# Optimization experiments

Measured on AMD Instinct MI355X. Metric: run time of the kernel, lower is better.

## Reference

```python
import jax, jax.numpy as jnp
import numpy as np

BN_EPS = 1e-5
MIN_DIST = 1e-10


def _conv_bn_relu(x, w, b, gamma, beta):
    # pointwise Conv1d (kernel=1) == per-point linear, then BatchNorm1d (training-mode
    # batch stats, biased variance, as torch does for normalization), then ReLU.
    y = jnp.einsum('oc,bcn->bon', w, x) + b[None, :, None]
    mu = y.mean(axis=(0, 2))
    var = y.var(axis=(0, 2))
    yn = (y - mu[None, :, None]) * jax.lax.rsqrt(var + BN_EPS)[None, :, None]
    return jax.nn.relu(yn * gamma[None, :, None] + beta[None, :, None])


def setup_inputs() -> dict:
    key = jax.random.key(0)
    ks = jax.random.split(key, 12)
    B, N1, N2, C1, C2 = 8, 8192, 2048, 128, 256
    in_ch = C1 + C2  # 384
    mlp = [256, 128]
    inp = {
        'xyz1': jax.random.normal(ks[0], (B, N1, 3), jnp.float32),
        'xyz2': jax.random.normal(ks[1], (B, N2, 3), jnp.float32),
        'points1': jax.random.normal(ks[2], (B, C1, N1), jnp.float32),
        'points2': jax.random.normal(ks[3], (B, C2, N2), jnp.float32),
    }
    last = in_ch
    for i, out_ch in enumerate(mlp):
        scale = 1.0 / np.sqrt(last)
        inp[f'w{i}'] = jax.random.uniform(ks[4 + 2 * i], (out_ch, last), jnp.float32, -scale, scale)
        inp[f'b{i}'] = jax.random.uniform(ks[5 + 2 * i], (out_ch,), jnp.float32, -scale, scale)
        inp[f'gamma{i}'] = jnp.ones((out_ch,), jnp.float32)
        inp[f'beta{i}'] = jnp.zeros((out_ch,), jnp.float32)
        last = out_ch
    return inp


def reference(xyz1, xyz2, points1, points2,
              w0, b0, gamma0, beta0, w1, b1, gamma1, beta1):
    # Euclidean distance matrix [B, N1, N2] (torch.cdist, p=2)
    sq = (jnp.sum(xyz1 * xyz1, -1)[:, :, None]
          + jnp.sum(xyz2 * xyz2, -1)[:, None, :]
          - 2.0 * jnp.einsum('bnd,bmd->bnm', xyz1, xyz2))
    dists = jnp.sqrt(jnp.maximum(sq, 0.0))
    # 3 smallest distances + indices (ascending, matching torch.topk largest=False)
    neg_d, knn_idx = jax.lax.top_k(-dists, 3)  # [B, N1, 3]
    knn_d = jnp.maximum(-neg_d, MIN_DIST)
    weights = 1.0 / knn_d
    weights = weights / jnp.sum(weights, axis=2, keepdims=True)  # [B, N1, 3]
    # gather neighbor features: points2 [B, C2, N2] -> [B, C2, N1, 3]
    knn_feats = jnp.take_along_axis(points2[:, :, None, :],
                                    knn_idx[:, None, :, :], axis=3)
    interpolated = jnp.sum(knn_feats * weights[:, None, :, :], axis=3)  # [B, C2, N1]
    new_points = jnp.concatenate([points1, interpolated], axis=1)  # [B, C1+C2, N1]
    new_points = _conv_bn_relu(new_points, w0, b0, gamma0, beta0)
    new_points = _conv_bn_relu(new_points, w1, b1, gamma1, beta1)
    return new_points
```

## Files before the change

### kernel.cpp

```cpp
#include <hip/hip_runtime.h>
#include <cstdint>

using u16 = unsigned short;
typedef short bf16x8 __attribute__((ext_vector_type(8)));
typedef float f32x4 __attribute__((ext_vector_type(4)));

__device__ __forceinline__ float bf2f(u16 h) {
    union { unsigned u; float f; } x;
    x.u = ((unsigned)h) << 16;
    return x.f;
}
__device__ __forceinline__ u16 f2bf(float f) {
    union { float f; unsigned u; } x;
    x.f = f;
    unsigned r = x.u + 0x7fffu + ((x.u >> 16) & 1u);
    return (u16)(r >> 16);
}

__global__ __launch_bounds__(256) void cvt_f32_bf16(const float* __restrict__ src,
                                                    u16* __restrict__ dst, int n) {
    int i = blockIdx.x * 256 + threadIdx.x;
    if (i < n) dst[i] = f2bf(src[i]);
}

__global__ __launch_bounds__(256) void transpose_to_bf16(const float* __restrict__ src,
                                                         u16* __restrict__ dst,
                                                         int C, int N, int dst_stride,
                                                         int col_off) {
    __shared__ float tile[32][33];
    int b = blockIdx.z;
    int n0 = blockIdx.x * 32, c0 = blockIdx.y * 32;
    int tx = threadIdx.x & 31, ty = threadIdx.x >> 5;
    const float* s = src + (long)b * C * N;
#pragma unroll
    for (int i = 0; i < 4; i++) {
        int c = ty + i * 8;
        tile[c][tx] = s[(long)(c0 + c) * N + n0 + tx];
    }
    __syncthreads();
    u16* d = dst + (long)b * N * dst_stride;
#pragma unroll
    for (int i = 0; i < 4; i++) {
        int n = ty + i * 8;
        d[(long)(n0 + n) * dst_stride + col_off + c0 + tx] = f2bf(tile[tx][n]);
    }
}

#define N1 8192
#define N2 2048
#define C2 256

__global__ __launch_bounds__(256) void knn_interp(const float* __restrict__ xyz1,
                                                  const float* __restrict__ xyz2,
                                                  const u16* __restrict__ P2T,
                                                  u16* __restrict__ X) {
    __shared__ float4 pts[N2];
    __shared__ float m_d[4][64][3];
    __shared__ int   m_i[4][64][3];
    __shared__ int   s_idx[64][3];
    __shared__ float s_w[64][3];
    int b = blockIdx.y;
    int n0 = blockIdx.x * 64;
    int tid = threadIdx.x;
    int ql = tid & 63;
    int part = tid >> 6;

    for (int j = tid; j < N2; j += 256) {
        float x = xyz2[((long)b * N2 + j) * 3 + 0];
        float y = xyz2[((long)b * N2 + j) * 3 + 1];
        float z = xyz2[((long)b * N2 + j) * 3 + 2];
        float nsq = __fadd_rn(__fadd_rn(__fmul_rn(x, x), __fmul_rn(y, y)), __fmul_rn(z, z));
        pts[j] = make_float4(x, y, z, nsq);
    }
    __syncthreads();

    int n = n0 + ql;
    float px = xyz1[((long)b * N1 + n) * 3 + 0];
    float py = xyz1[((long)b * N1 + n) * 3 + 1];
    float pz = xyz1[((long)b * N1 + n) * 3 + 2];
    float psq = __fadd_rn(__fadd_rn(__fmul_rn(px, px), __fmul_rn(py, py)), __fmul_rn(pz, pz));

    float b0 = 1e30f, b1 = 1e30f, b2 = 1e30f;
    int i0 = 0, i1 = 0, i2 = 0;
    int jbeg = part * (N2 / 4);
#pragma unroll 8
    for (int jj = 0; jj < N2 / 4; jj++) {
        int j = jbeg + jj;
        float4 p = pts[j];
        float dot = __fadd_rn(__fadd_rn(__fmul_rn(px, p.x), __fmul_rn(py, p.y)),
                              __fmul_rn(pz, p.z));
        float sq = __fsub_rn(__fadd_rn(psq, p.w), __fmul_rn(2.0f, dot));
        if (sq < b2) {
            if (sq < b1) {
                b2 = b1; i2 = i1;
                if (sq < b0) { b1 = b0; i1 = i0; b0 = sq; i0 = j; }
                else         { b1 = sq; i1 = j; }
            } else { b2 = sq; i2 = j; }
        }
    }
    m_d[part][ql][0] = b0; m_d[part][ql][1] = b1; m_d[part][ql][2] = b2;
    m_i[part][ql][0] = i0; m_i[part][ql][1] = i1; m_i[part][ql][2] = i2;
    __syncthreads();

    if (tid < 64) {
        float c0 = 1e30f, c1 = 1e30f, c2 = 1e30f;
        int a0 = 0x7fffffff, a1 = 0x7fffffff, a2 = 0x7fffffff;
#pragma unroll
        for (int pp = 0; pp < 4; pp++) {
#pragma unroll
            for (int k = 0; k < 3; k++) {
                float d = m_d[pp][tid][k];
                int ix = m_i[pp][tid][k];
                if (d < c2 || (d == c2 && ix < a2)) {
                    if (d < c1 || (d == c1 && ix < a1)) {
                        c2 = c1; a2 = a1;
                        if (d < c0 || (d == c0 && ix < a0)) { c1 = c0; a1 = a0; c0 = d; a0 = ix; }
                        else                                { c1 = d; a1 = ix; }
                    } else { c2 = d; a2 = ix; }
                }
            }
        }
        float e0 = sqrtf(fmaxf(c0, 0.0f));
        float e1 = sqrtf(fmaxf(c1, 0.0f));
        float e2 = sqrtf(fmaxf(c2, 0.0f));
        float kd0 = fmaxf(e0, 1e-10f), kd1 = fmaxf(e1, 1e-10f), kd2 = fmaxf(e2, 1e-10f);
        float w0 = __fdiv_rn(1.0f, kd0), w1 = __fdiv_rn(1.0f, kd1), w2 = __fdiv_rn(1.0f, kd2);
        float wsum = __fadd_rn(__fadd_rn(w0, w1), w2);
        s_idx[tid][0] = a0; s_idx[tid][1] = a1; s_idx[tid][2] = a2;
        s_w[tid][0] = __fdiv_rn(w0, wsum);
        s_w[tid][1] = __fdiv_rn(w1, wsum);
        s_w[tid][2] = __fdiv_rn(w2, wsum);
    }
    __syncthreads();

    int l = tid & 63;
    const u16* base = P2T + (long)b * N2 * C2;
    for (int p = part; p < 64; p += 4) {
        int j0 = s_idx[p][0], j1 = s_idx[p][1], j2 = s_idx[p][2];
        float f0 = s_w[p][0], f1 = s_w[p][1], f2 = s_w[p][2];
        ushort4 r0 = *(const ushort4*)&base[(long)j0 * C2 + l * 4];
        ushort4 r1 = *(const ushort4*)&base[(long)j1 * C2 + l * 4];
        ushort4 r2 = *(const ushort4*)&base[(long)j2 * C2 + l * 4];
        ushort4 o;
        {
            float acc = __fadd_rn(__fadd_rn(__fmul_rn(bf2f(r0.x), f0), __fmul_rn(bf2f(r1.x), f1)),
                                  __fmul_rn(bf2f(r2.x), f2));
            o.x = f2bf(acc);
        }
        {
            float acc = __fadd_rn(__fadd_rn(__fmul_rn(bf2f(r0.y), f0), __fmul_rn(bf2f(r1.y), f1)),
                                  __fmul_rn(bf2f(r2.y), f2));
            o.y = f2bf(acc);
        }
        {
            float acc = __fadd_rn(__fadd_rn(__fmul_rn(bf2f(r0.z), f0), __fmul_rn(bf2f(r1.z), f1)),
                                  __fmul_rn(bf2f(r2.z), f2));
            o.z = f2bf(acc);
        }
        {
            float acc = __fadd_rn(__fadd_rn(__fmul_rn(bf2f(r0.w), f0), __fmul_rn(bf2f(r1.w), f1)),
                                  __fmul_rn(bf2f(r2.w), f2));
            o.w = f2bf(acc);
        }
        *(ushort4*)&X[(long)(b * N1 + n0 + p) * 384 + 128 + l * 4] = o;
    }
}

template <int KDIM, bool BN_IN, bool OUT_BF16>
__global__ __launch_bounds__(256) void gemm_bn(const u16* __restrict__ A,
                                               const u16* __restrict__ Bw,
                                               const float* __restrict__ bias,
                                               const float* __restrict__ g_in_sum,
                                               const float* __restrict__ g_in_ssq,
                                               const float* __restrict__ gamma_in,
                                               const float* __restrict__ beta_in,
                                               void* __restrict__ Yout, int Ntot,
                                               float* __restrict__ g_out_sum,
                                               float* __restrict__ g_out_ssq) {
    __shared__ __align__(16) u16 Al[128 * 40];
    __shared__ __align__(16) u16 Bl[128 * 40];
    __shared__ float s_stats[256];
    __shared__ float s_scale[BN_IN ? KDIM : 2];
    __shared__ float s_shift[BN_IN ? KDIM : 2];

    int tid = threadIdx.x;
    long s0 = (long)blockIdx.x * 128;
    int o0 = blockIdx.y * 128;

    s_stats[tid < 256 ? tid : 0] = 0.0f;
    if constexpr (BN_IN) {
        for (int k = tid; k < KDIM; k += 256) {
            float mu = g_in_sum[k] * (1.0f / 65536.0f);
            float var = g_in_ssq[k] * (1.0f / 65536.0f) - mu * mu;
            float rs = rsqrtf(var + 1e-5f);
            float sc = gamma_in[k] * rs;
            s_scale[k] = sc;
            s_shift[k] = beta_in[k] - mu * sc;
        }
    }
    int wid = tid >> 6, lane = tid & 63;
    int wm = wid >> 1, wn = wid & 1;
    int q = lane >> 4, l16 = lane & 15;

    f32x4 acc[4][4];
#pragma unroll
    for (int mi = 0; mi < 4; mi++)
#pragma unroll
        for (int ni = 0; ni < 4; ni++) acc[mi][ni] = (f32x4){0.f, 0.f, 0.f, 0.f};
    __syncthreads();

    for (int kt = 0; kt < KDIM; kt += 32) {
#pragma unroll
        for (int cc = 0; cc < 2; cc++) {
            int ci = tid + cc * 256;
            int row = ci >> 2;
            int kc = (ci & 3) << 3;
            union { uint4 u; u16 h[8]; } va;
            va.u = *(const uint4*)(A + (s0 + row) * KDIM + kt + kc);
            if constexpr (BN_IN) {
#pragma unroll
                for (int j = 0; j < 8; j++) {
                    float f = bf2f(va.h[j]);
                    f = fmaxf(fmaf(f, s_scale[kt + kc + j], s_shift[kt + kc + j]), 0.0f);
                    va.h[j] = f2bf(f);
                }
            }
            *(uint4*)&Al[row * 40 + kc] = va.u;
            *(uint4*)&Bl[row * 40 + kc] = *(const uint4*)(Bw + (long)(o0 + row) * KDIM + kt + kc);
        }
        __syncthreads();
        bf16x8 af[4], bfr[4];
#pragma unroll
        for (int mi = 0; mi < 4; mi++)
            af[mi] = *(const bf16x8*)&Al[(wm * 64 + mi * 16 + l16) * 40 + q * 8];
#pragma unroll
        for (int ni = 0; ni < 4; ni++)
            bfr[ni] = *(const bf16x8*)&Bl[(wn * 64 + ni * 16 + l16) * 40 + q * 8];
#pragma unroll
        for (int mi = 0; mi < 4; mi++)
#pragma unroll
            for (int ni = 0; ni < 4; ni++)
                acc[mi][ni] = __builtin_amdgcn_mfma_f32_16x16x32_bf16(af[mi], bfr[ni],
                                                                      acc[mi][ni], 0, 0, 0);
        __syncthreads();
    }

#pragma unroll
    for (int ni = 0; ni < 4; ni++) {
        int coll = wn * 64 + ni * 16 + l16;
        int col = o0 + coll;
        float bz = bias[col];
        float s1 = 0.0f, s2 = 0.0f;
#pragma unroll
        for (int mi = 0; mi < 4; mi++) {
#pragma unroll
            for (int r = 0; r < 4; r++) {
                float v = acc[mi][ni][r] + bz;
                s1 += v;
                s2 += v * v;
                long row = s0 + wm * 64 + mi * 16 + q * 4 + r;
                if constexpr (OUT_BF16)
                    ((u16*)Yout)[row * Ntot + col] = f2bf(v);
                else
                    ((float*)Yout)[row * Ntot + col] = v;
            }
        }
        s1 += __shfl_xor(s1, 16, 64);
        s1 += __shfl_xor(s1, 32, 64);
        s2 += __shfl_xor(s2, 16, 64);
        s2 += __shfl_xor(s2, 32, 64);
        if (q == 0) {
            atomicAdd(&s_stats[coll], s1);
            atomicAdd(&s_stats[128 + coll], s2);
        }
    }
    __syncthreads();
    if (tid < 128) {
        atomicAdd(&g_out_sum[o0 + tid], s_stats[tid]);
        atomicAdd(&g_out_ssq[o0 + tid], s_stats[128 + tid]);
    }
}

__global__ __launch_bounds__(256) void finalize_k(const float* __restrict__ Y1,
                                                  const float* __restrict__ g_sum,
                                                  const float* __restrict__ g_ssq,
                                                  const float* __restrict__ gamma,
                                                  const float* __restrict__ beta,
                                                  float* __restrict__ out) {
    __shared__ float s_scale[128], s_shift[128];
    int tid = threadIdx.x;
    if (tid < 128) {
        float mu = g_sum[tid] * (1.0f / 65536.0f);
        float var = g_ssq[tid] * (1.0f / 65536.0f) - mu * mu;
        float rs = rsqrtf(var + 1e-5f);
        float sc = gamma[tid] * rs;
        s_scale[tid] = sc;
        s_shift[tid] = beta[tid] - mu * sc;
    }
    __syncthreads();
    long s = (long)blockIdx.x * 256 + tid;
    int b = (int)(s >> 13);
    int n = (int)(s & 8191);
    const float* yrow = Y1 + s * 128;
    float* obase = out + (long)b * 128 * 8192 + n;
#pragma unroll 8
    for (int o = 0; o < 128; o++) {
        float v = fmaxf(fmaf(yrow[o], s_scale[o], s_shift[o]), 0.0f);
        obase[(long)o * 8192] = v;
    }
}

extern "C" void kernel_launch(void* const* d_in, const int* in_sizes, int n_in,
                              void* d_out, int out_size, void* d_ws, size_t ws_size,
                              hipStream_t stream) {
    const float* xyz1   = (const float*)d_in[0];
    const float* xyz2   = (const float*)d_in[1];
    const float* points1 = (const float*)d_in[2];
    const float* points2 = (const float*)d_in[3];
    const float* w0 = (const float*)d_in[4];
    const float* b0 = (const float*)d_in[5];
    const float* gamma0 = (const float*)d_in[6];
    const float* beta0 = (const float*)d_in[7];
    const float* w1 = (const float*)d_in[8];
    const float* b1 = (const float*)d_in[9];
    const float* gamma1 = (const float*)d_in[10];
    const float* beta1 = (const float*)d_in[11];
    float* out = (float*)d_out;

    char* ws = (char*)d_ws;
    u16* X    = (u16*)(ws + 0);
    u16* P2T  = (u16*)(ws + 50331648);
    u16* w0b  = (u16*)(ws + 58720256);
    u16* w1b  = (u16*)(ws + 58916864);
    u16* Y0   = (u16*)(ws + 58982400);
    float* Y1 = (float*)(ws + 92536832);
    float* stats = (float*)(ws + 126091264);
    if (ws_size < 126094336) return;
    float* gsum0 = stats;
    float* gss0  = stats + 256;
    float* gsum1 = stats + 512;
    float* gss1  = stats + 640;

    hipMemsetAsync(stats, 0, 768 * sizeof(float), stream);
    cvt_f32_bf16<<<384, 256, 0, stream>>>(w0, w0b, 98304);
    cvt_f32_bf16<<<128, 256, 0, stream>>>(w1, w1b, 32768);
    transpose_to_bf16<<<dim3(256, 4, 8), 256, 0, stream>>>(points1, X, 128, 8192, 384, 0);
    transpose_to_bf16<<<dim3(64, 8, 8), 256, 0, stream>>>(points2, P2T, 256, 2048, 256, 0);
    knn_interp<<<dim3(128, 8), 256, 0, stream>>>(xyz1, xyz2, P2T, X);
    gemm_bn<384, false, true><<<dim3(512, 2), 256, 0, stream>>>(
        X, w0b, b0, nullptr, nullptr, nullptr, nullptr, Y0, 256, gsum0, gss0);
    gemm_bn<256, true, false><<<dim3(512, 1), 256, 0, stream>>>(
        Y0, w1b, b1, gsum0, gss0, gamma0, beta0, Y1, 128, gsum1, gss1);
    finalize_k<<<256, 256, 0, stream>>>(Y1, gsum1, gss1, gamma1, beta1, out);
}
```

Baseline: 281.9 us.

## Fuse prep kernels, precompute xyz2 norms, widen KNN blocks, store Y1 as bf16

Merges the weight conversions, the stats memset and a new xyz2 preprocessing step (pre-scaled coordinates plus squared norm) into one prep kernel. The KNN kernel now reads that precomputed array from global memory instead of staging it in LDS. It uses 512 threads split into 8 parts and replaces the branchy top-3 insert with branchless selects. The second GEMM writes bf16 instead of fp32, and finalize reads it with vectorized loads, which halves the intermediate traffic at some cost in precision.

Result: no change. 284.8 us (+1.0%).

```diff
diff --git a/kernel.cpp b/kernel.cpp
--- a/kernel.cpp
+++ b/kernel.cpp
@@ -17,10 +17,32 @@
     return (u16)(r >> 16);
 }
 
-__global__ __launch_bounds__(256) void cvt_f32_bf16(const float* __restrict__ src,
-                                                    u16* __restrict__ dst, int n) {
-    int i = blockIdx.x * 256 + threadIdx.x;
-    if (i < n) dst[i] = f2bf(src[i]);
+#define N1 8192
+#define N2 2048
+#define C2 256
+
+__global__ __launch_bounds__(256) void prep_misc(const float* __restrict__ w0,
+                                                 const float* __restrict__ w1,
+                                                 const float* __restrict__ xyz2,
+                                                 u16* __restrict__ w0b,
+                                                 u16* __restrict__ w1b,
+                                                 float4* __restrict__ P2P,
+                                                 float* __restrict__ stats) {
+    int bid = blockIdx.x, tid = threadIdx.x;
+    if (bid < 384) {
+        int i = bid * 256 + tid;
+        w0b[i] = f2bf(w0[i]);
+    } else if (bid < 512) {
+        int i = (bid - 384) * 256 + tid;
+        w1b[i] = f2bf(w1[i]);
+    } else if (bid < 576) {
+        int i = (bid - 512) * 256 + tid;
+        float x = xyz2[i * 3 + 0], y = xyz2[i * 3 + 1], z = xyz2[i * 3 + 2];
+        float nsq = __fadd_rn(__fadd_rn(__fmul_rn(x, x), __fmul_rn(y, y)), __fmul_rn(z, z));
+        P2P[i] = make_float4(-2.0f * x, -2.0f * y, -2.0f * z, nsq);
+    } else {
+        for (int i = tid; i < 768; i += 256) stats[i] = 0.0f;
+    }
 }
 
 __global__ __launch_bounds__(256) void transpose_to_bf16(const float* __restrict__ src,
@@ -46,33 +68,19 @@
     }
 }
 
-#define N1 8192
-#define N2 2048
-#define C2 256
-
-__global__ __launch_bounds__(256) void knn_interp(const float* __restrict__ xyz1,
-                                                  const float* __restrict__ xyz2,
+__global__ __launch_bounds__(512) void knn_interp(const float* __restrict__ xyz1,
+                                                  const float4* __restrict__ P2P,
                                                   const u16* __restrict__ P2T,
                                                   u16* __restrict__ X) {
-    __shared__ float4 pts[N2];
-    __shared__ float m_d[4][64][3];
-    __shared__ int   m_i[4][64][3];
+    __shared__ float m_d[8][64][3];
+    __shared__ int   m_i[8][64][3];
     __shared__ int   s_idx[64][3];
     __shared__ float s_w[64][3];
     int b = blockIdx.y;
     int n0 = blockIdx.x * 64;
     int tid = threadIdx.x;
     int ql = tid & 63;
-    int part = tid >> 6;
-
-    for (int j = tid; j < N2; j += 256) {
-        float x = xyz2[((long)b * N2 + j) * 3 + 0];
-        float y = xyz2[((long)b * N2 + j) * 3 + 1];
-        float z = xyz2[((long)b * N2 + j) * 3 + 2];
-        float nsq = __fadd_rn(__fadd_rn(__fmul_rn(x, x), __fmul_rn(y, y)), __fmul_rn(z, z));
-        pts[j] = make_float4(x, y, z, nsq);
-    }
-    __syncthreads();
+    int part = __builtin_amdgcn_readfirstlane(tid >> 6);
 
     int n = n0 + ql;
     float px = xyz1[((long)b * N1 + n) * 3 + 0];
@@ -80,23 +88,23 @@
     float pz = xyz1[((long)b * N1 + n) * 3 + 2];
     float psq = __fadd_rn(__fadd_rn(__fmul_rn(px, px), __fmul_rn(py, py)), __fmul_rn(pz, pz));
 
+    const float4* __restrict__ pp = P2P + (long)b * N2 + part * (N2 / 8);
+    int jbeg = part * (N2 / 8);
     float b0 = 1e30f, b1 = 1e30f, b2 = 1e30f;
     int i0 = 0, i1 = 0, i2 = 0;
-    int jbeg = part * (N2 / 4);
-#pragma unroll 8
-    for (int jj = 0; jj < N2 / 4; jj++) {
+#pragma unroll 4
+    for (int jj = 0; jj < N2 / 8; jj++) {
+        float4 p = pp[jj];
+        float u = __fadd_rn(__fadd_rn(__fmul_rn(p.x, px), __fmul_rn(p.y, py)),
+                            __fmul_rn(p.z, pz));
+        float sq = __fadd_rn(__fadd_rn(psq, p.w), u);
         int j = jbeg + jj;
-        float4 p = pts[j];
-        float dot = __fadd_rn(__fadd_rn(__fmul_rn(px, p.x), __fmul_rn(py, p.y)),
-                              __fmul_rn(pz, p.z));
-        float sq = __fsub_rn(__fadd_rn(psq, p.w), __fmul_rn(2.0f, dot));
-        if (sq < b2) {
-            if (sq < b1) {
-                b2 = b1; i2 = i1;
-                if (sq < b0) { b1 = b0; i1 = i0; b0 = sq; i0 = j; }
-                else         { b1 = sq; i1 = j; }
-            } else { b2 = sq; i2 = j; }
-        }
+        bool c0 = sq < b0, c1 = sq < b1, c2 = sq < b2;
+        float t1 = c0 ? b0 : sq;  int ti1 = c0 ? i0 : j;
+        b0 = c0 ? sq : b0;        i0 = c0 ? j : i0;
+        float t2 = c1 ? b1 : t1;  int ti2 = c1 ? i1 : ti1;
+        b1 = c1 ? t1 : b1;        i1 = c1 ? ti1 : i1;
+        b2 = c2 ? t2 : b2;        i2 = c2 ? ti2 : i2;
     }
     m_d[part][ql][0] = b0; m_d[part][ql][1] = b1; m_d[part][ql][2] = b2;
     m_i[part][ql][0] = i0; m_i[part][ql][1] = i1; m_i[part][ql][2] = i2;
@@ -106,11 +114,11 @@
         float c0 = 1e30f, c1 = 1e30f, c2 = 1e30f;
         int a0 = 0x7fffffff, a1 = 0x7fffffff, a2 = 0x7fffffff;
 #pragma unroll
-        for (int pp = 0; pp < 4; pp++) {
+        for (int pp2 = 0; pp2 < 8; pp2++) {
 #pragma unroll
             for (int k = 0; k < 3; k++) {
-                float d = m_d[pp][tid][k];
-                int ix = m_i[pp][tid][k];
+                float d = m_d[pp2][tid][k];
+                int ix = m_i[pp2][tid][k];
                 if (d < c2 || (d == c2 && ix < a2)) {
                     if (d < c1 || (d == c1 && ix < a1)) {
                         c2 = c1; a2 = a1;
@@ -135,33 +143,21 @@
 
     int l = tid & 63;
     const u16* base = P2T + (long)b * N2 * C2;
-    for (int p = part; p < 64; p += 4) {
+    for (int p = part; p < 64; p += 8) {
         int j0 = s_idx[p][0], j1 = s_idx[p][1], j2 = s_idx[p][2];
         float f0 = s_w[p][0], f1 = s_w[p][1], f2 = s_w[p][2];
         ushort4 r0 = *(const ushort4*)&base[(long)j0 * C2 + l * 4];
         ushort4 r1 = *(const ushort4*)&base[(long)j1 * C2 + l * 4];
         ushort4 r2 = *(const ushort4*)&base[(long)j2 * C2 + l * 4];
         ushort4 o;
-        {
-            float acc = __fadd_rn(__fadd_rn(__fmul_rn(bf2f(r0.x), f0), __fmul_rn(bf2f(r1.x), f1)),
-                                  __fmul_rn(bf2f(r2.x), f2));
-            o.x = f2bf(acc);
-        }
-        {
-            float acc = __fadd_rn(__fadd_rn(__fmul_rn(bf2f(r0.y), f0), __fmul_rn(bf2f(r1.y), f1)),
-                                  __fmul_rn(bf2f(r2.y), f2));
-            o.y = f2bf(acc);
-        }
-        {
-            float acc = __fadd_rn(__fadd_rn(__fmul_rn(bf2f(r0.z), f0), __fmul_rn(bf2f(r1.z), f1)),
-                                  __fmul_rn(bf2f(r2.z), f2));
-            o.z = f2bf(acc);
-        }
-        {
-            float acc = __fadd_rn(__fadd_rn(__fmul_rn(bf2f(r0.w), f0), __fmul_rn(bf2f(r1.w), f1)),
-                                  __fmul_rn(bf2f(r2.w), f2));
-            o.w = f2bf(acc);
-        }
+        o.x = f2bf(__fadd_rn(__fadd_rn(__fmul_rn(bf2f(r0.x), f0), __fmul_rn(bf2f(r1.x), f1)),
+                             __fmul_rn(bf2f(r2.x), f2)));
+        o.y = f2bf(__fadd_rn(__fadd_rn(__fmul_rn(bf2f(r0.y), f0), __fmul_rn(bf2f(r1.y), f1)),
+                             __fmul_rn(bf2f(r2.y), f2)));
+        o.z = f2bf(__fadd_rn(__fadd_rn(__fmul_rn(bf2f(r0.z), f0), __fmul_rn(bf2f(r1.z), f1)),
+                             __fmul_rn(bf2f(r2.z), f2)));
+        o.w = f2bf(__fadd_rn(__fadd_rn(__fmul_rn(bf2f(r0.w), f0), __fmul_rn(bf2f(r1.w), f1)),
+                             __fmul_rn(bf2f(r2.w), f2)));
         *(ushort4*)&X[(long)(b * N1 + n0 + p) * 384 + 128 + l * 4] = o;
     }
 }
@@ -281,7 +277,7 @@
     }
 }
 
-__global__ __launch_bounds__(256) void finalize_k(const float* __restrict__ Y1,
+__global__ __launch_bounds__(256) void finalize_k(const u16* __restrict__ Y1,
                                                   const float* __restrict__ g_sum,
                                                   const float* __restrict__ g_ssq,
                                                   const float* __restrict__ gamma,
@@ -301,20 +297,26 @@
     long s = (long)blockIdx.x * 256 + tid;
     int b = (int)(s >> 13);
     int n = (int)(s & 8191);
-    const float* yrow = Y1 + s * 128;
+    const u16* yrow = Y1 + s * 128;
     float* obase = out + (long)b * 128 * 8192 + n;
-#pragma unroll 8
-    for (int o = 0; o < 128; o++) {
-        float v = fmaxf(fmaf(yrow[o], s_scale[o], s_shift[o]), 0.0f);
-        obase[(long)o * 8192] = v;
+#pragma unroll
+    for (int oc = 0; oc < 128; oc += 8) {
+        union { uint4 u; u16 h[8]; } va;
+        va.u = *(const uint4*)&yrow[oc];
+#pragma unroll
+        for (int k = 0; k < 8; k++) {
+            int o = oc + k;
+            float v = fmaxf(fmaf(bf2f(va.h[k]), s_scale[o], s_shift[o]), 0.0f);
+            obase[(long)o * 8192] = v;
+        }
     }
 }
 
 extern "C" void kernel_launch(void* const* d_in, const int* in_sizes, int n_in,
                               void* d_out, int out_size, void* d_ws, size_t ws_size,
                               hipStream_t stream) {
-    const float* xyz1   = (const float*)d_in[0];
-    const float* xyz2   = (const float*)d_in[1];
+    const float* xyz1    = (const float*)d_in[0];
+    const float* xyz2    = (const float*)d_in[1];
     const float* points1 = (const float*)d_in[2];
     const float* points2 = (const float*)d_in[3];
     const float* w0 = (const float*)d_in[4];
@@ -328,12 +330,13 @@
     float* out = (float*)d_out;
 
     char* ws = (char*)d_ws;
-    u16* X    = (u16*)(ws + 0);
-    u16* P2T  = (u16*)(ws + 50331648);
-    u16* w0b  = (u16*)(ws + 58720256);
-    u16* w1b  = (u16*)(ws + 58916864);
-    u16* Y0   = (u16*)(ws + 58982400);
-    float* Y1 = (float*)(ws + 92536832);
+    u16* X      = (u16*)(ws + 0);
+    u16* P2T    = (u16*)(ws + 50331648);
+    u16* w0b    = (u16*)(ws + 58720256);
+    u16* w1b    = (u16*)(ws + 58916864);
+    u16* Y0     = (u16*)(ws + 58982400);
+    float4* P2P = (float4*)(ws + 92536832);
+    u16* Y1b    = (u16*)(ws + 92798976);
     float* stats = (float*)(ws + 126091264);
     if (ws_size < 126094336) return;
     float* gsum0 = stats;
@@ -341,15 +344,13 @@
     float* gsum1 = stats + 512;
     float* gss1  = stats + 640;
 
-    hipMemsetAsync(stats, 0, 768 * sizeof(float), stream);
-    cvt_f32_bf16<<<384, 256, 0, stream>>>(w0, w0b, 98304);
-    cvt_f32_bf16<<<128, 256, 0, stream>>>(w1, w1b, 32768);
+    prep_misc<<<577, 256, 0, stream>>>(w0, w1, xyz2, w0b, w1b, P2P, stats);
     transpose_to_bf16<<<dim3(256, 4, 8), 256, 0, stream>>>(points1, X, 128, 8192, 384, 0);
     transpose_to_bf16<<<dim3(64, 8, 8), 256, 0, stream>>>(points2, P2T, 256, 2048, 256, 0);
-    knn_interp<<<dim3(128, 8), 256, 0, stream>>>(xyz1, xyz2, P2T, X);
+    knn_interp<<<dim3(128, 8), 512, 0, stream>>>(xyz1, P2P, P2T, X);
     gemm_bn<384, false, true><<<dim3(512, 2), 256, 0, stream>>>(
         X, w0b, b0, nullptr, nullptr, nullptr, nullptr, Y0, 256, gsum0, gss0);
-    gemm_bn<256, true, false><<<dim3(512, 1), 256, 0, stream>>>(
-        Y0, w1b, b1, gsum0, gss0, gamma0, beta0, Y1, 128, gsum1, gss1);
-    finalize_k<<<256, 256, 0, stream>>>(Y1, gsum1, gss1, gamma1, beta1, out);
-}
+    gemm_bn<256, true, true><<<dim3(512, 1), 256, 0, stream>>>(
+        Y0, w1b, b1, gsum0, gss0, gamma0, beta0, Y1b, 128, gsum1, gss1);
+    finalize_k<<<256, 256, 0, stream>>>(Y1b, gsum1, gss1, gamma1, beta1, out);
+}
```
